# Optimization experiments

Measured on AMD Instinct MI355X. Metric: run time of the kernel, lower is better.

## Reference

```python
import jax, jax.numpy as jnp
import numpy as np

MAX_PTS = 512     # _MAX_POINTS_PER_BOX
MIN_PTS = 4       # _MIN_POINTS_FOR_NET


def setup_inputs() -> dict:
    key = jax.random.key(0)
    ks = jax.random.split(key, 8)
    N, A = 131072, 1024
    # LiDAR-like cloud over a 100m x 100m plot, heights up to 30m
    points = jax.random.uniform(ks[0], (N, 3)) * jnp.array([100.0, 100.0, 30.0])
    # anchors: (x, y, z_c, w, l, h); z_c is unused by the box test in the source
    cxy = jax.random.uniform(ks[1], (A, 2)) * 100.0
    wl = 2.0 + jax.random.uniform(ks[2], (A, 2)) * 4.0      # 2..6 m footprint
    h = 20.0 + jax.random.uniform(ks[3], (A, 1)) * 15.0     # 20..35 m tall
    anchors = jnp.concatenate([cxy, jnp.zeros((A, 1)), wl, h], axis=-1)
    W1 = jax.random.normal(ks[4], (3, 64)) * 0.3
    W2 = jax.random.normal(ks[5], (64, 128)) * 0.1
    Wc = jax.random.normal(ks[6], (128, 1)) * 0.1
    Wr = jax.random.normal(ks[7], (128, 4)) * 0.1
    return {
        'points': points, 'anchors': anchors,
        'W1': W1, 'b1': jnp.zeros(64), 'W2': W2, 'b2': jnp.zeros(128),
        'Wc': Wc, 'bc': jnp.zeros(1), 'Wr': Wr, 'br': jnp.zeros(4),
    }


def reference(points, anchors, W1, b1, W2, b2, Wc, bc, Wr, br):
    # points: (N,3)  anchors: (A,6) = (x, y, z_c, w, l, h)
    N = points.shape[0]
    x, y = anchors[:, 0], anchors[:, 1]
    w, l, h = anchors[:, 3], anchors[:, 4], anchors[:, 5]
    px, py, pz = points[:, 0], points[:, 1], points[:, 2]
    # point-in-box test, (A, N)  -- mirrors _subsample_points_in_box
    inside = ((px[None] >= (x - w / 2)[:, None]) & (px[None] <= (x + w / 2)[:, None]) &
              (py[None] >= (y - l / 2)[:, None]) & (py[None] <= (y + l / 2)[:, None]) &
              (pz[None] >= 0.0) & (pz[None] <= h[:, None]))
    count = inside.sum(-1)                                   # (A,)
    # first MAX_PTS inside-points per anchor (deterministic subsample)
    score = jnp.where(inside, -jnp.arange(N, dtype=jnp.float32)[None], -jnp.inf)
    _, idx = jax.lax.top_k(score, MAX_PTS)                   # (A, K)
    # repeat-padding as in _pad_windows_to_batch: cycle through the n points
    pos = jnp.arange(MAX_PTS)[None] % jnp.maximum(count, 1)[:, None]
    gidx = jnp.take_along_axis(idx, pos, axis=1)             # (A, K)
    pts = points[gidx]                                       # (A, K, 3)
    # normalize xy relative to anchor center (z untouched)
    pts = pts - jnp.stack([x, y, jnp.zeros_like(x)], -1)[:, None, :]
    # stage1 PointNet head: per-point MLP -> max-pool -> cls/reg linears
    f = jax.nn.relu(pts @ W1 + b1)
    f = jax.nn.relu(f @ W2 + b2)                             # (A, K, 128)
    g = f.max(axis=1)                                        # (A, 128)
    cls = g @ Wc + bc                                        # (A, 1)
    reg = g @ Wr + br                                        # (A, 4)
    # anchors with < MIN_PTS points get zeroed outputs (as in the source)
    valid = (count >= MIN_PTS)[:, None].astype(pts.dtype)
    return jnp.concatenate([cls, reg], axis=-1) * valid      # (A, 5)
```

## Files before the change

### kernel.cpp

```cpp
#include <hip/hip_runtime.h>
#include <hip/hip_bf16.h>
#include <stdint.h>

#define NPTS   131072
#define NANCH  1024
#define GRID   25
#define NCELL  (GRID*GRID)
#define CINV   0.25f
#define MAXP   512
#define MINP   4
#define IDXCAP 1024
#define HB     128
#define PPB    (NPTS/HB)

typedef __attribute__((ext_vector_type(8))) short bf16x8;
typedef __attribute__((ext_vector_type(4))) float f32x4;

__device__ __forceinline__ int cell_of(float px, float py) {
    int cx = (int)(px * CINV); cx = cx < 0 ? 0 : (cx > GRID-1 ? GRID-1 : cx);
    int cy = (int)(py * CINV); cy = cy < 0 ? 0 : (cy > GRID-1 ? GRID-1 : cy);
    return cy * GRID + cx;
}

__device__ __forceinline__ unsigned short f2bf(float f) {
    union { float f; uint32_t u; } v; v.f = f;
    return (unsigned short)((v.u + 0x7fff + ((v.u >> 16) & 1)) >> 16);
}


__global__ __launch_bounds__(256) void k_hist(const float* __restrict__ pts,
                                              int* __restrict__ blockhist) {
    __shared__ int lh[NCELL];
    const int b = blockIdx.x, tid = threadIdx.x;
    for (int i = tid; i < NCELL; i += 256) lh[i] = 0;
    __syncthreads();
    const int base = b * PPB;
    #pragma unroll
    for (int k = 0; k < PPB/256; k++) {
        int i = base + k*256 + tid;
        atomicAdd(&lh[cell_of(pts[3*i], pts[3*i+1])], 1);
    }
    __syncthreads();
    for (int i = tid; i < NCELL; i += 256) blockhist[b*NCELL + i] = lh[i];
}

__global__ __launch_bounds__(1024) void k_scan(const int* __restrict__ blockhist,
                                               int* __restrict__ blockpre,
                                               int* __restrict__ cstart) {
    __shared__ int sc[1024];
    const int c = threadIdx.x;
    int acc = 0;
    if (c < NCELL) {
        #pragma unroll 8
        for (int b = 0; b < HB; b++) {
            int v = blockhist[b*NCELL + c];
            blockpre[b*NCELL + c] = acc;
            acc += v;
        }
    }
    sc[c] = (c < NCELL) ? acc : 0;
    __syncthreads();
    for (int off = 1; off < 1024; off <<= 1) {
        int x = (c >= off) ? sc[c - off] : 0;
        __syncthreads();
        sc[c] += x;
        __syncthreads();
    }
    if (c < NCELL) cstart[c] = sc[c] - acc;
    if (c == NCELL-1) cstart[NCELL] = sc[c];
}

__global__ __launch_bounds__(256) void k_scatter(const float* __restrict__ pts,
                                                 const int* __restrict__ blockpre,
                                                 const int* __restrict__ cstart,
                                                 float4* __restrict__ binned) {
    __shared__ int lh[NCELL];
    __shared__ int lbase[NCELL];
    const int b = blockIdx.x, tid = threadIdx.x;
    for (int i = tid; i < NCELL; i += 256) {
        lh[i] = 0;
        lbase[i] = cstart[i] + blockpre[b*NCELL + i];
    }
    __syncthreads();
    const int base = b * PPB;
    #pragma unroll
    for (int k = 0; k < PPB/256; k++) {
        int i = base + k*256 + tid;
        float px = pts[3*i], py = pts[3*i+1], pz = pts[3*i+2];
        int c = cell_of(px, py);
        int r = atomicAdd(&lh[c], 1);
        binned[lbase[c] + r] = make_float4(px, py, pz, __int_as_float(i));
    }
}


__launch_bounds__(256, 4)
__global__ void k_main(const float* __restrict__ pts,
                       const float* __restrict__ anch,
                       const float* __restrict__ W1, const float* __restrict__ b1,
                       const float* __restrict__ W2, const float* __restrict__ b2,
                       const float* __restrict__ Wc, const float* __restrict__ bc,
                       const float* __restrict__ Wr, const float* __restrict__ br,
                       const float4* __restrict__ binned,
                       const int* __restrict__ cstart,
                       float* __restrict__ out) {
    __shared__ float spx[MAXP], spy[MAXP], spz[MAXP];
    __shared__ int   sidx[IDXCAP];
    __shared__ unsigned short h1b[32*64];
    __shared__ unsigned short w2t[128*64];
    __shared__ float w1s[3][64];
    __shared__ float b1s[64];
    __shared__ float gmax2[128];
    __shared__ int   s_cnt;

    const int a    = blockIdx.x;
    const int tid  = threadIdx.x;
    const int lane = tid & 63;
    const int wv   = tid >> 6;

    const float ax = anch[6*a],   ay = anch[6*a+1];
    const float w  = anch[6*a+3], l  = anch[6*a+4], hh = anch[6*a+5];
    const float hw = w * 0.5f, hl = l * 0.5f;
    const float x0 = ax - hw, x1 = ax + hw, y0 = ay - hl, y1 = ay + hl;

    if (tid == 0) s_cnt = 0;
    if (tid < 64) {
        w1s[0][tid] = W1[tid]; w1s[1][tid] = W1[64+tid]; w1s[2][tid] = W1[128+tid];
        b1s[tid] = b1[tid];
    }
    {
        const int col = tid >> 1, k0 = (tid & 1) * 32;
        #pragma unroll
        for (int kk = 0; kk < 32; kk += 2) {
            int k = k0 + kk;
            float f0 = W2[k*128 + col], f1 = W2[(k+1)*128 + col];
            uint32_t pk = (uint32_t)f2bf(f0) | ((uint32_t)f2bf(f1) << 16);
            int idx = (col*64 + k) ^ ((col & 7) << 3);
            *(uint32_t*)&w2t[idx] = pk;
        }
    }
    __syncthreads();

    int cx0 = (int)floorf(x0 * CINV); if (cx0 < 0) cx0 = 0;
    int cx1 = (int)floorf(x1 * CINV); if (cx1 > GRID-1) cx1 = GRID-1;
    int cy0 = (int)floorf(y0 * CINV); if (cy0 < 0) cy0 = 0;
    int cy1 = (int)floorf(y1 * CINV); if (cy1 > GRID-1) cy1 = GRID-1;

    for (int cy = cy0; cy <= cy1; cy++)
        for (int cx = cx0; cx <= cx1; cx++) {
            int c = cy * GRID + cx;
            int p0 = cstart[c], p1 = cstart[c+1];
            for (int base = p0; base < p1; base += 256) {
                int i = base + tid;
                if (i < p1) {
                    float4 P = binned[i];
                    float px = P.x, py = P.y, pz = P.z;
                    bool ins = (px >= x0) & (px <= x1) & (py >= y0) & (py <= y1)
                             & (pz >= 0.f) & (pz <= hh);
                    if (ins) {
                        int pos = atomicAdd(&s_cnt, 1);
                        if (pos < MAXP)   { spx[pos] = px - ax; spy[pos] = py - ay; spz[pos] = pz; }
                        if (pos < IDXCAP) sidx[pos] = __float_as_int(P.w);
                    }
                }
            }
        }
    __syncthreads();
    const int cnt = s_cnt;

    if (cnt < MINP) {
        if (tid < 5) out[5*a + tid] = 0.f;
        return;
    }

    if (cnt > MAXP) {
        for (int i = cnt + tid; i < IDXCAP; i += 256) sidx[i] = 0x7fffffff;
        __syncthreads();
        for (int k = 2; k <= IDXCAP; k <<= 1) {
            for (int j = k >> 1; j > 0; j >>= 1) {
                #pragma unroll
                for (int e = 0; e < IDXCAP/256; e++) {
                    int i = tid + e*256;
                    int partner = i ^ j;
                    if (partner > i) {
                        int va = sidx[i], vb = sidx[partner];
                        bool up = ((i & k) == 0);
                        if ((va > vb) == up) { sidx[i] = vb; sidx[partner] = va; }
                    }
                }
                __syncthreads();
            }
        }
        for (int i = tid; i < MAXP; i += 256) {
            int idx = sidx[i];
            spx[i] = pts[3*idx]   - ax;
            spy[i] = pts[3*idx+1] - ay;
            spz[i] = pts[3*idx+2];
        }
        __syncthreads();
    }

    const int gathered = cnt < MAXP ? cnt : MAXP;
    const int padded   = (gathered + 31) & ~31;
    for (int i = gathered + tid; i < padded; i += 256) {
        spx[i] = spx[0]; spy[i] = spy[0]; spz[i] = spz[0];
    }
    __syncthreads();

    bf16x8 b00, b01, b10, b11;
    {
        const int l15 = lane & 15, kb = (lane >> 4) * 8;
        int c0 = wv*16 + l15, c1 = (wv+4)*16 + l15;
        int i00 = (c0*64 +  0 + kb) ^ ((c0 & 7) << 3);
        int i01 = (c0*64 + 32 + kb) ^ ((c0 & 7) << 3);
        int i10 = (c1*64 +  0 + kb) ^ ((c1 & 7) << 3);
        int i11 = (c1*64 + 32 + kb) ^ ((c1 & 7) << 3);
        b00 = *(const bf16x8*)&w2t[i00];
        b01 = *(const bf16x8*)&w2t[i01];
        b10 = *(const bf16x8*)&w2t[i10];
        b11 = *(const bf16x8*)&w2t[i11];
    }

    float gm0 = -INFINITY, gm1 = -INFINITY;
    const int pairid = tid & 31;
    const int rbase  = tid >> 5;
    const int l15 = lane & 15, kb = (lane >> 4) * 8;

    for (int pb = 0; pb < padded; pb += 32) {
        #pragma unroll
        for (int pass = 0; pass < 4; pass++) {
            int row = pass*8 + rbase;
            int p = pb + row;
            float qx = spx[p], qy = spy[p], qz = spz[p];
            int d0 = pairid * 2;
            float v0 = fmaf(qz, w1s[2][d0],   fmaf(qy, w1s[1][d0],   fmaf(qx, w1s[0][d0],   b1s[d0])));
            float v1 = fmaf(qz, w1s[2][d0+1], fmaf(qy, w1s[1][d0+1], fmaf(qx, w1s[0][d0+1], b1s[d0+1])));
            v0 = fmaxf(v0, 0.f); v1 = fmaxf(v1, 0.f);
            uint32_t pk = (uint32_t)f2bf(v0) | ((uint32_t)f2bf(v1) << 16);
            int idx = (row*64 + d0) ^ ((row & 7) << 3);
            *(uint32_t*)&h1b[idx] = pk;
        }
        __syncthreads();

        int r0 = l15, r1 = 16 + l15;
        int a00i = (r0*64 +  0 + kb) ^ ((r0 & 7) << 3);
        int a01i = (r0*64 + 32 + kb) ^ ((r0 & 7) << 3);
        int a10i = (r1*64 +  0 + kb) ^ ((r1 & 7) << 3);
        int a11i = (r1*64 + 32 + kb) ^ ((r1 & 7) << 3);
        bf16x8 a00 = *(const bf16x8*)&h1b[a00i];
        bf16x8 a01 = *(const bf16x8*)&h1b[a01i];
        bf16x8 a10 = *(const bf16x8*)&h1b[a10i];
        bf16x8 a11 = *(const bf16x8*)&h1b[a11i];

        f32x4 z = {0.f, 0.f, 0.f, 0.f};
        f32x4 c;
        c = __builtin_amdgcn_mfma_f32_16x16x32_bf16(a00, b00, z, 0, 0, 0);
        c = __builtin_amdgcn_mfma_f32_16x16x32_bf16(a01, b01, c, 0, 0, 0);
        gm0 = fmaxf(gm0, fmaxf(fmaxf(c[0], c[1]), fmaxf(c[2], c[3])));
        c = __builtin_amdgcn_mfma_f32_16x16x32_bf16(a10, b00, z, 0, 0, 0);
        c = __builtin_amdgcn_mfma_f32_16x16x32_bf16(a11, b01, c, 0, 0, 0);
        gm0 = fmaxf(gm0, fmaxf(fmaxf(c[0], c[1]), fmaxf(c[2], c[3])));
        c = __builtin_amdgcn_mfma_f32_16x16x32_bf16(a00, b10, z, 0, 0, 0);
        c = __builtin_amdgcn_mfma_f32_16x16x32_bf16(a01, b11, c, 0, 0, 0);
        gm1 = fmaxf(gm1, fmaxf(fmaxf(c[0], c[1]), fmaxf(c[2], c[3])));
        c = __builtin_amdgcn_mfma_f32_16x16x32_bf16(a10, b10, z, 0, 0, 0);
        c = __builtin_amdgcn_mfma_f32_16x16x32_bf16(a11, b11, c, 0, 0, 0);
        gm1 = fmaxf(gm1, fmaxf(fmaxf(c[0], c[1]), fmaxf(c[2], c[3])));
        __syncthreads();
    }

    gm0 = fmaxf(gm0, __shfl_xor(gm0, 16)); gm0 = fmaxf(gm0, __shfl_xor(gm0, 32));
    gm1 = fmaxf(gm1, __shfl_xor(gm1, 16)); gm1 = fmaxf(gm1, __shfl_xor(gm1, 32));
    if (lane < 16) {
        gmax2[wv*16     + lane] = gm0;
        gmax2[(wv+4)*16 + lane] = gm1;
    }
    __syncthreads();
    if (tid < 128) gmax2[tid] = fmaxf(gmax2[tid] + b2[tid], 0.f);
    __syncthreads();

    if (tid < 5) {
        const float* Wv; float bias; int stride;
        if (tid == 0) { Wv = Wc;            bias = bc[0];      stride = 1; }
        else          { Wv = Wr + (tid-1);  bias = br[tid-1];  stride = 4; }
        float acc = bias;
        for (int i = 0; i < 128; i++) acc = fmaf(gmax2[i], Wv[i*stride], acc);
        out[5*a + tid] = acc;
    }
}


extern "C" void kernel_launch(void* const* d_in, const int* in_sizes, int n_in,
                              void* d_out, int out_size, void* d_ws, size_t ws_size,
                              hipStream_t stream) {
    const float* pts  = (const float*)d_in[0];
    const float* anch = (const float*)d_in[1];
    const float* W1   = (const float*)d_in[2];
    const float* b1   = (const float*)d_in[3];
    const float* W2   = (const float*)d_in[4];
    const float* b2   = (const float*)d_in[5];
    const float* Wc   = (const float*)d_in[6];
    const float* bc   = (const float*)d_in[7];
    const float* Wr   = (const float*)d_in[8];
    const float* br   = (const float*)d_in[9];
    float* out = (float*)d_out;

    char* ws = (char*)d_ws;
    float4* binned    = (float4*)ws;
    int*    blockhist = (int*)(ws + (size_t)NPTS*16);
    int*    blockpre  = blockhist + HB*NCELL;
    int*    cstart    = blockpre  + HB*NCELL;

    k_hist   <<<HB, 256, 0, stream>>>(pts, blockhist);
    k_scan   <<<1, 1024, 0, stream>>>(blockhist, blockpre, cstart);
    k_scatter<<<HB, 256, 0, stream>>>(pts, blockpre, cstart, binned);
    k_main   <<<NANCH, 256, 0, stream>>>(pts, anch, W1, b1, W2, b2, Wc, bc, Wr, br,
                                         binned, cstart, out);
}
```

Measured before the change: 109.5 us.

## Precompute W2 bf16 globally, reuse hist ranks, ballot-compact gathers, 64-row MLP tiles

Converts W2 to transposed bf16 once inside the scan kernel, and each k_main block loads its MFMA B fragments from global memory into registers instead of rebuilding a 16KB LDS copy. The histogram kernel now stores each point's cell and rank so the scatter kernel skips recomputing cells and the shared atomics. In-box point collection uses wave ballot plus popcount with one atomic per wave. The MLP loop processes 64 points per tile, halving barrier rounds at the cost of more padding. Together these cut per-block setup work, shared-atomic contention and synchronisation, and the smaller LDS footprint may allow more resident blocks.

```diff
diff --git a/kernel.cpp b/kernel.cpp
--- a/kernel.cpp
+++ b/kernel.cpp
@@ -29,7 +29,8 @@
 
 
 __global__ __launch_bounds__(256) void k_hist(const float* __restrict__ pts,
-                                              int* __restrict__ blockhist) {
+                                              int* __restrict__ blockhist,
+                                              int* __restrict__ cellrank) {
     __shared__ int lh[NCELL];
     const int b = blockIdx.x, tid = threadIdx.x;
     for (int i = tid; i < NCELL; i += 256) lh[i] = 0;
@@ -38,7 +39,9 @@
     #pragma unroll
     for (int k = 0; k < PPB/256; k++) {
         int i = base + k*256 + tid;
-        atomicAdd(&lh[cell_of(pts[3*i], pts[3*i+1])], 1);
+        int c = cell_of(pts[3*i], pts[3*i+1]);
+        int r = atomicAdd(&lh[c], 1);
+        cellrank[i] = c | (r << 10);
     }
     __syncthreads();
     for (int i = tid; i < NCELL; i += 256) blockhist[b*NCELL + i] = lh[i];
@@ -46,7 +49,9 @@
 
 __global__ __launch_bounds__(1024) void k_scan(const int* __restrict__ blockhist,
                                                int* __restrict__ blockpre,
-                                               int* __restrict__ cstart) {
+                                               int* __restrict__ cstart,
+                                               const float* __restrict__ W2,
+                                               unsigned short* __restrict__ w2tg) {
     __shared__ int sc[1024];
     const int c = threadIdx.x;
     int acc = 0;
@@ -57,6 +62,16 @@
             blockpre[b*NCELL + c] = acc;
             acc += v;
         }
+    } else if (c >= 640 && c < 896) {
+        int u = c - 640;
+        int col = u >> 1, ks = (u & 1) * 32;
+        #pragma unroll
+        for (int kk = 0; kk < 32; kk += 2) {
+            int k = ks + kk;
+            uint32_t pk = (uint32_t)f2bf(W2[k*128 + col])
+                        | ((uint32_t)f2bf(W2[(k+1)*128 + col]) << 16);
+            *(uint32_t*)&w2tg[col*64 + k] = pk;
+        }
     }
     sc[c] = (c < NCELL) ? acc : 0;
     __syncthreads();
@@ -71,25 +86,23 @@
 }
 
 __global__ __launch_bounds__(256) void k_scatter(const float* __restrict__ pts,
+                                                 const int* __restrict__ cellrank,
                                                  const int* __restrict__ blockpre,
                                                  const int* __restrict__ cstart,
                                                  float4* __restrict__ binned) {
-    __shared__ int lh[NCELL];
     __shared__ int lbase[NCELL];
     const int b = blockIdx.x, tid = threadIdx.x;
-    for (int i = tid; i < NCELL; i += 256) {
-        lh[i] = 0;
+    for (int i = tid; i < NCELL; i += 256)
         lbase[i] = cstart[i] + blockpre[b*NCELL + i];
-    }
     __syncthreads();
     const int base = b * PPB;
     #pragma unroll
     for (int k = 0; k < PPB/256; k++) {
         int i = base + k*256 + tid;
-        float px = pts[3*i], py = pts[3*i+1], pz = pts[3*i+2];
-        int c = cell_of(px, py);
-        int r = atomicAdd(&lh[c], 1);
-        binned[lbase[c] + r] = make_float4(px, py, pz, __int_as_float(i));
+        int v = cellrank[i];
+        int c = v & 1023, r = v >> 10;
+        binned[lbase[c] + r] = make_float4(pts[3*i], pts[3*i+1], pts[3*i+2],
+                                           __int_as_float(i));
     }
 }
 
@@ -98,16 +111,16 @@
 __global__ void k_main(const float* __restrict__ pts,
                        const float* __restrict__ anch,
                        const float* __restrict__ W1, const float* __restrict__ b1,
-                       const float* __restrict__ W2, const float* __restrict__ b2,
+                       const float* __restrict__ b2,
                        const float* __restrict__ Wc, const float* __restrict__ bc,
                        const float* __restrict__ Wr, const float* __restrict__ br,
+                       const unsigned short* __restrict__ w2tg,
                        const float4* __restrict__ binned,
                        const int* __restrict__ cstart,
                        float* __restrict__ out) {
     __shared__ float spx[MAXP], spy[MAXP], spz[MAXP];
     __shared__ int   sidx[IDXCAP];
-    __shared__ unsigned short h1b[32*64];
-    __shared__ unsigned short w2t[128*64];
+    __shared__ unsigned short h1b[64*64];
     __shared__ float w1s[3][64];
     __shared__ float b1s[64];
     __shared__ float gmax2[128];
@@ -117,27 +130,27 @@
     const int tid  = threadIdx.x;
     const int lane = tid & 63;
     const int wv   = tid >> 6;
+    const int l15  = lane & 15;
+    const int kb   = (lane >> 4) * 8;
 
     const float ax = anch[6*a],   ay = anch[6*a+1];
     const float w  = anch[6*a+3], l  = anch[6*a+4], hh = anch[6*a+5];
     const float hw = w * 0.5f, hl = l * 0.5f;
     const float x0 = ax - hw, x1 = ax + hw, y0 = ay - hl, y1 = ay + hl;
 
+    bf16x8 b00, b01, b10, b11;
+    {
+        const int c0 = wv*16 + l15, c1 = c0 + 64;
+        b00 = *(const bf16x8*)&w2tg[c0*64 + kb];
+        b01 = *(const bf16x8*)&w2tg[c0*64 + 32 + kb];
+        b10 = *(const bf16x8*)&w2tg[c1*64 + kb];
+        b11 = *(const bf16x8*)&w2tg[c1*64 + 32 + kb];
+    }
+
     if (tid == 0) s_cnt = 0;
     if (tid < 64) {
         w1s[0][tid] = W1[tid]; w1s[1][tid] = W1[64+tid]; w1s[2][tid] = W1[128+tid];
         b1s[tid] = b1[tid];
-    }
-    {
-        const int col = tid >> 1, k0 = (tid & 1) * 32;
-        #pragma unroll
-        for (int kk = 0; kk < 32; kk += 2) {
-            int k = k0 + kk;
-            float f0 = W2[k*128 + col], f1 = W2[(k+1)*128 + col];
-            uint32_t pk = (uint32_t)f2bf(f0) | ((uint32_t)f2bf(f1) << 16);
-            int idx = (col*64 + k) ^ ((col & 7) << 3);
-            *(uint32_t*)&w2t[idx] = pk;
-        }
     }
     __syncthreads();
 
@@ -152,16 +165,21 @@
             int p0 = cstart[c], p1 = cstart[c+1];
             for (int base = p0; base < p1; base += 256) {
                 int i = base + tid;
+                bool ins = false;
+                float4 P;
                 if (i < p1) {
-                    float4 P = binned[i];
-                    float px = P.x, py = P.y, pz = P.z;
-                    bool ins = (px >= x0) & (px <= x1) & (py >= y0) & (py <= y1)
-                             & (pz >= 0.f) & (pz <= hh);
-                    if (ins) {
-                        int pos = atomicAdd(&s_cnt, 1);
-                        if (pos < MAXP)   { spx[pos] = px - ax; spy[pos] = py - ay; spz[pos] = pz; }
-                        if (pos < IDXCAP) sidx[pos] = __float_as_int(P.w);
-                    }
+                    P = binned[i];
+                    ins = (P.x >= x0) & (P.x <= x1) & (P.y >= y0) & (P.y <= y1)
+                        & (P.z >= 0.f) & (P.z <= hh);
+                }
+                unsigned long long m = __ballot(ins);
+                int wbase;
+                if (lane == 0) wbase = atomicAdd(&s_cnt, __popcll(m));
+                wbase = __shfl(wbase, 0);
+                if (ins) {
+                    int pos = wbase + __popcll(m & ((1ull << lane) - 1ull));
+                    if (pos < MAXP)   { spx[pos] = P.x - ax; spy[pos] = P.y - ay; spz[pos] = P.z; }
+                    if (pos < IDXCAP) sidx[pos] = __float_as_int(P.w);
                 }
             }
         }
@@ -201,35 +219,20 @@
     }
 
     const int gathered = cnt < MAXP ? cnt : MAXP;
-    const int padded   = (gathered + 31) & ~31;
+    const int padded   = (gathered + 63) & ~63;
     for (int i = gathered + tid; i < padded; i += 256) {
         spx[i] = spx[0]; spy[i] = spy[0]; spz[i] = spz[0];
     }
     __syncthreads();
 
-    bf16x8 b00, b01, b10, b11;
-    {
-        const int l15 = lane & 15, kb = (lane >> 4) * 8;
-        int c0 = wv*16 + l15, c1 = (wv+4)*16 + l15;
-        int i00 = (c0*64 +  0 + kb) ^ ((c0 & 7) << 3);
-        int i01 = (c0*64 + 32 + kb) ^ ((c0 & 7) << 3);
-        int i10 = (c1*64 +  0 + kb) ^ ((c1 & 7) << 3);
-        int i11 = (c1*64 + 32 + kb) ^ ((c1 & 7) << 3);
-        b00 = *(const bf16x8*)&w2t[i00];
-        b01 = *(const bf16x8*)&w2t[i01];
-        b10 = *(const bf16x8*)&w2t[i10];
-        b11 = *(const bf16x8*)&w2t[i11];
-    }
-
     float gm0 = -INFINITY, gm1 = -INFINITY;
     const int pairid = tid & 31;
-    const int rbase  = tid >> 5;
-    const int l15 = lane & 15, kb = (lane >> 4) * 8;
-
-    for (int pb = 0; pb < padded; pb += 32) {
+    const int rowg   = tid >> 5;
+
+    for (int pb = 0; pb < padded; pb += 64) {
         #pragma unroll
-        for (int pass = 0; pass < 4; pass++) {
-            int row = pass*8 + rbase;
+        for (int pass = 0; pass < 8; pass++) {
+            int row = pass*8 + rowg;
             int p = pb + row;
             float qx = spx[p], qy = spy[p], qz = spz[p];
             int d0 = pairid * 2;
@@ -242,30 +245,22 @@
         }
         __syncthreads();
 
-        int r0 = l15, r1 = 16 + l15;
-        int a00i = (r0*64 +  0 + kb) ^ ((r0 & 7) << 3);
-        int a01i = (r0*64 + 32 + kb) ^ ((r0 & 7) << 3);
-        int a10i = (r1*64 +  0 + kb) ^ ((r1 & 7) << 3);
-        int a11i = (r1*64 + 32 + kb) ^ ((r1 & 7) << 3);
-        bf16x8 a00 = *(const bf16x8*)&h1b[a00i];
-        bf16x8 a01 = *(const bf16x8*)&h1b[a01i];
-        bf16x8 a10 = *(const bf16x8*)&h1b[a10i];
-        bf16x8 a11 = *(const bf16x8*)&h1b[a11i];
-
-        f32x4 z = {0.f, 0.f, 0.f, 0.f};
-        f32x4 c;
-        c = __builtin_amdgcn_mfma_f32_16x16x32_bf16(a00, b00, z, 0, 0, 0);
-        c = __builtin_amdgcn_mfma_f32_16x16x32_bf16(a01, b01, c, 0, 0, 0);
-        gm0 = fmaxf(gm0, fmaxf(fmaxf(c[0], c[1]), fmaxf(c[2], c[3])));
-        c = __builtin_amdgcn_mfma_f32_16x16x32_bf16(a10, b00, z, 0, 0, 0);
-        c = __builtin_amdgcn_mfma_f32_16x16x32_bf16(a11, b01, c, 0, 0, 0);
-        gm0 = fmaxf(gm0, fmaxf(fmaxf(c[0], c[1]), fmaxf(c[2], c[3])));
-        c = __builtin_amdgcn_mfma_f32_16x16x32_bf16(a00, b10, z, 0, 0, 0);
-        c = __builtin_amdgcn_mfma_f32_16x16x32_bf16(a01, b11, c, 0, 0, 0);
-        gm1 = fmaxf(gm1, fmaxf(fmaxf(c[0], c[1]), fmaxf(c[2], c[3])));
-        c = __builtin_amdgcn_mfma_f32_16x16x32_bf16(a10, b10, z, 0, 0, 0);
-        c = __builtin_amdgcn_mfma_f32_16x16x32_bf16(a11, b11, c, 0, 0, 0);
-        gm1 = fmaxf(gm1, fmaxf(fmaxf(c[0], c[1]), fmaxf(c[2], c[3])));
+        #pragma unroll
+        for (int mt = 0; mt < 4; mt++) {
+            int r = mt*16 + l15;
+            int ai0 = (r*64 +      kb) ^ ((r & 7) << 3);
+            int ai1 = (r*64 + 32 + kb) ^ ((r & 7) << 3);
+            bf16x8 a0 = *(const bf16x8*)&h1b[ai0];
+            bf16x8 a1 = *(const bf16x8*)&h1b[ai1];
+            f32x4 z = {0.f, 0.f, 0.f, 0.f};
+            f32x4 c;
+            c = __builtin_amdgcn_mfma_f32_16x16x32_bf16(a0, b00, z, 0, 0, 0);
+            c = __builtin_amdgcn_mfma_f32_16x16x32_bf16(a1, b01, c, 0, 0, 0);
+            gm0 = fmaxf(gm0, fmaxf(fmaxf(c[0], c[1]), fmaxf(c[2], c[3])));
+            c = __builtin_amdgcn_mfma_f32_16x16x32_bf16(a0, b10, z, 0, 0, 0);
+            c = __builtin_amdgcn_mfma_f32_16x16x32_bf16(a1, b11, c, 0, 0, 0);
+            gm1 = fmaxf(gm1, fmaxf(fmaxf(c[0], c[1]), fmaxf(c[2], c[3])));
+        }
         __syncthreads();
     }
 
@@ -306,14 +301,16 @@
     float* out = (float*)d_out;
 
     char* ws = (char*)d_ws;
-    float4* binned    = (float4*)ws;
-    int*    blockhist = (int*)(ws + (size_t)NPTS*16);
-    int*    blockpre  = blockhist + HB*NCELL;
-    int*    cstart    = blockpre  + HB*NCELL;
-
-    k_hist   <<<HB, 256, 0, stream>>>(pts, blockhist);
-    k_scan   <<<1, 1024, 0, stream>>>(blockhist, blockpre, cstart);
-    k_scatter<<<HB, 256, 0, stream>>>(pts, blockpre, cstart, binned);
-    k_main   <<<NANCH, 256, 0, stream>>>(pts, anch, W1, b1, W2, b2, Wc, bc, Wr, br,
-                                         binned, cstart, out);
-}
+    float4*         binned    = (float4*)ws;
+    int*            blockhist = (int*)(ws + (size_t)NPTS*16);
+    int*            blockpre  = blockhist + HB*NCELL;
+    int*            cstart    = blockpre  + HB*NCELL;
+    int*            cellrank  = cstart + 1024;
+    unsigned short* w2tg      = (unsigned short*)(cellrank + NPTS);
+
+    k_hist   <<<HB, 256, 0, stream>>>(pts, blockhist, cellrank);
+    k_scan   <<<1, 1024, 0, stream>>>(blockhist, blockpre, cstart, W2, w2tg);
+    k_scatter<<<HB, 256, 0, stream>>>(pts, cellrank, blockpre, cstart, binned);
+    k_main   <<<NANCH, 256, 0, stream>>>(pts, anch, W1, b1, b2, Wc, bc, Wr, br,
+                                         w2tg, binned, cstart, out);
+}
```

Result: no change. 109.4 us (-0.1%).
